# Kernel optimization log

Hardware: AMD Instinct MI355X
Metric: run time of the kernel (lower is better)

The kernel has to match this reference:

```python
import jax, jax.numpy as jnp
import numpy as np
from jax import lax

C = 41  # class_size
B = 1024
T = 1024

def setup_inputs() -> dict:
    key = jax.random.key(0)
    k1, k2, k3, k4 = jax.random.split(key, 4)
    x = jax.random.normal(k1, (B, T, C), dtype=jnp.float32)
    # torchcrf initializes transitions uniform in [-0.1, 0.1]
    start_transitions = jax.random.uniform(k2, (C,), minval=-0.1, maxval=0.1, dtype=jnp.float32)
    end_transitions = jax.random.uniform(k3, (C,), minval=-0.1, maxval=0.1, dtype=jnp.float32)
    transitions = jax.random.uniform(k4, (C, C), minval=-0.1, maxval=0.1, dtype=jnp.float32)
    return {"x": x, "start_transitions": start_transitions,
            "end_transitions": end_transitions, "transitions": transitions}

def reference(x, start_transitions, end_transitions, transitions):
    # Viterbi decode (torchcrf CRF.decode, batch_first, no mask).
    # x: [B, T, C] emissions. Returns best tag sequence [B, T] int32.
    emis_t = jnp.swapaxes(x, 0, 1)  # [T, B, C]
    score0 = start_transitions[None, :] + emis_t[0]  # [B, C]

    def fwd_step(score, emit):
        # score [B, C] (prev tag), emit [B, C] (next tag)
        # next_score[b, i, j] = score[b, i] + trans[i, j] + emit[b, j]
        ns = score[:, :, None] + transitions[None, :, :] + emit[:, None, :]
        best_prev = jnp.argmax(ns, axis=1).astype(jnp.int32)  # [B, C]
        return jnp.max(ns, axis=1), best_prev

    final_score, history = lax.scan(fwd_step, score0, emis_t[1:])  # history [T-1, B, C]
    final_score = final_score + end_transitions[None, :]
    last_tag = jnp.argmax(final_score, axis=1).astype(jnp.int32)  # [B]

    def back_step(tag, idx_t):
        # idx_t [B, C]: best previous tag given current tag
        prev = jnp.take_along_axis(idx_t, tag[:, None], axis=1)[:, 0]
        return prev, prev

    _, tags_prefix = lax.scan(back_step, last_tag, history, reverse=True)  # [T-1, B]
    tags = jnp.concatenate([tags_prefix, last_tag[None, :]], axis=0)  # [T, B]
    return jnp.swapaxes(tags, 0, 1)  # [B, T]
```

## Files before the change

### kernel.cpp

```cpp
#include <hip/hip_runtime.h>
#include <stdint.h>

#define NCLASS 41
#define TLEN   1024
#define NBATCH 1024
#define BP_STRIDE 41944
#define NTRANS (NCLASS * NCLASS)
#define NEGINF (-3.0e38f)
#define MASK41 ((1ull << NCLASS) - 1)

__device__ __forceinline__ float wave_max_bcast(float x) {
    int xi = __float_as_int(x);
    int t;
    t = __builtin_amdgcn_update_dpp(xi, xi, 0x111, 0xf, 0xf, false);
    x = fmaxf(x, __int_as_float(t)); xi = __float_as_int(x);
    t = __builtin_amdgcn_update_dpp(xi, xi, 0x112, 0xf, 0xf, false);
    x = fmaxf(x, __int_as_float(t)); xi = __float_as_int(x);
    t = __builtin_amdgcn_update_dpp(xi, xi, 0x114, 0xf, 0xf, false);
    x = fmaxf(x, __int_as_float(t)); xi = __float_as_int(x);
    t = __builtin_amdgcn_update_dpp(xi, xi, 0x118, 0xf, 0xf, false);
    x = fmaxf(x, __int_as_float(t)); xi = __float_as_int(x);
    t = __builtin_amdgcn_update_dpp(xi, xi, 0x142, 0xf, 0xf, false);
    x = fmaxf(x, __int_as_float(t)); xi = __float_as_int(x);
    t = __builtin_amdgcn_update_dpp(xi, xi, 0x143, 0xf, 0xf, false);
    x = fmaxf(x, __int_as_float(t));
    return __int_as_float(__builtin_amdgcn_readlane(__float_as_int(x), 63));
}

#define RDLANE(v, l) __int_as_float(__builtin_amdgcn_readlane(__float_as_int(v), (l)))

__global__ __launch_bounds__(64, 1) void crf_forward(
    const float* __restrict__ x,
    const float* __restrict__ start_t,
    const float* __restrict__ end_t,
    const float* __restrict__ trans,
    uint8_t* __restrict__ bp,
    int* __restrict__ out)
{
    __shared__ float tl[NTRANS + 32];

    const int b = blockIdx.x;
    const int j = threadIdx.x;
    const int jc = (j < NCLASS) ? j : (NCLASS - 1);

    float mx = NEGINF, mn = 3.0e38f;
    for (int k = j; k < NTRANS; k += 64) {
        float v = trans[k];
        tl[k] = v;
        mx = fmaxf(mx, v);
        mn = fminf(mn, v);
    }
    __syncthreads();
    const float Dmax = wave_max_bcast(mx);
    const float Dmin = -wave_max_bcast(-mn);
    const float D = Dmax - Dmin;

    const float* xb = x + (size_t)b * TLEN * NCLASS;
    uint8_t* bpb = bp + (size_t)b * BP_STRIDE;

    float score = start_t[jc] + xb[jc];
    float thr = wave_max_bcast(score) - D;

    auto step = [&](float e, int boff) {
        unsigned long long me =
            __ballot(score >= thr) & MASK41;
        int cnt = __popcll(me);
        int i1 = __ffsll(me) - 1;
        int i2 = 63 - __clzll(me);
        float s1 = RDLANE(score, i1);
        float s2 = RDLANE(score, i2);
        float t1 = tl[i1 * NCLASS + jc];
        float t2 = tl[i2 * NCLASS + jc];
        float v1 = s1 + t1;
        float v2 = s2 + t2;
        bool c = v2 > v1;
        float best = c ? v2 : v1;
        int bidx = c ? i2 : i1;
        if (__builtin_expect(cnt >= 3, 0)) {
            unsigned long long mr =
                me & ~((1ull << i1) | (1ull << i2));
            if (__builtin_expect(cnt <= 4, 1)) {
                int i3 = __ffsll(mr) - 1;
                int i4 = 63 - __clzll(mr);
                float s3 = RDLANE(score, i3);
                float s4 = RDLANE(score, i4);
                float v3 = s3 + tl[i3 * NCLASS + jc];
                float v4 = s4 + tl[i4 * NCLASS + jc];
                best = v1; bidx = i1;
                if (v3 > best) { best = v3; bidx = i3; }
                if (v4 > best) { best = v4; bidx = i4; }
                if (v2 > best) { best = v2; bidx = i2; }
            } else {
                best = NEGINF; bidx = 0;
                unsigned long long mm = me;
                while (mm) {
                    int ic = __ffsll(mm) - 1; mm &= mm - 1;
                    float sc = RDLANE(score, ic);
                    float vc = sc + tl[ic * NCLASS + jc];
                    if (vc > best) { best = vc; bidx = ic; }
                }
            }
        }
        bpb[boff] = (uint8_t)bidx;
        score = best + e;
        thr = wave_max_bcast(score) - D;
    };

    int eoff = 1 * NCLASS + jc;
    float e0 = xb[eoff];
    float e1 = xb[eoff + NCLASS];
    float e2 = xb[eoff + 2 * NCLASS];
    float e3 = xb[eoff + 3 * NCLASS];
    eoff += 4 * NCLASS;
    int boff = jc;

    int t0 = 1;
    for (; t0 + 7 <= TLEN - 4; t0 += 4) {
        step(e0, boff);              e0 = xb[eoff];
        step(e1, boff + NCLASS);     e1 = xb[eoff + NCLASS];
        step(e2, boff + 2 * NCLASS); e2 = xb[eoff + 2 * NCLASS];
        step(e3, boff + 3 * NCLASS); e3 = xb[eoff + 3 * NCLASS];
        eoff += 4 * NCLASS;
        boff += 4 * NCLASS;
    }
    step(e0, boff);              e0 = xb[eoff];
    step(e1, boff + NCLASS);     e1 = xb[eoff + NCLASS];
    step(e2, boff + 2 * NCLASS); e2 = xb[eoff + 2 * NCLASS];
    step(e3, boff + 3 * NCLASS);
    boff += 4 * NCLASS;
    step(e0, boff);
    step(e1, boff + NCLASS);
    step(e2, boff + 2 * NCLASS);

    float fs = score + end_t[jc];
    int idx = j;
#pragma unroll
    for (int off = 32; off >= 1; off >>= 1) {
        float ov = __shfl_xor(fs, off);
        int oi = __shfl_xor(idx, off);
        if (ov > fs || (ov == fs && oi < idx)) { fs = ov; idx = oi; }
    }
    if (j == 0) out[(size_t)b * TLEN + (TLEN - 1)] = idx;
}

__global__ __launch_bounds__(1024) void crf_backtrack(
    const uint8_t* __restrict__ bp,
    int* __restrict__ out)
{
    __shared__ uint8_t bpl[BP_STRIDE];
    __shared__ int maps[16][NCLASS];
    __shared__ int entry[16];

    const int b = blockIdx.x;
    const int tid = threadIdx.x;
    const int w = tid >> 6;
    const int lane = tid & 63;

    {
        const uint32_t* src = (const uint32_t*)(bp + (size_t)b * BP_STRIDE);
        uint32_t* dst = (uint32_t*)bpl;
        for (int i = tid; i < BP_STRIDE / 4; i += 1024) dst[i] = src[i];
    }
    __syncthreads();

    const int cs = w * 64;
    const int ce = min(cs + 64, TLEN - 1);
    const int L = ce - cs;

    {
        int xx = (lane < NCLASS) ? lane : 0;
        for (int t = ce; t > cs; --t)
            xx = bpl[(t - 1) * NCLASS + xx];
        if (lane < NCLASS) maps[w][lane] = xx;
    }
    __syncthreads();

    if (tid == 0) {
        int cur = out[(size_t)b * TLEN + (TLEN - 1)];
        for (int ww = 15; ww >= 0; --ww) {
            entry[ww] = cur;
            cur = maps[ww][cur];
        }
    }
    __syncthreads();

    {
        int xx = entry[w];
        int cap = 0;
        for (int k = 0; k < L; ++k) {
            xx = bpl[(ce - 1 - k) * NCLASS + xx];
            if (k == lane) cap = xx;
        }
        if (lane < L) out[(size_t)b * TLEN + (ce - 1 - lane)] = cap;
    }
}

extern "C" void kernel_launch(void* const* d_in, const int* in_sizes, int n_in,
                              void* d_out, int out_size, void* d_ws, size_t ws_size,
                              hipStream_t stream) {
    const float* x       = (const float*)d_in[0];
    const float* start_t = (const float*)d_in[1];
    const float* end_t   = (const float*)d_in[2];
    const float* trans   = (const float*)d_in[3];
    int* out = (int*)d_out;
    uint8_t* bp = (uint8_t*)d_ws;

    crf_forward<<<NBATCH, 64, 0, stream>>>(x, start_t, end_t, trans, bp, out);
    crf_backtrack<<<NBATCH, 1024, 0, stream>>>(bp, out);
}
```

Measured before the change: 261.0 us.

## Derive next-step pruning threshold from current max and emission max off critical path

The pruning threshold for the next step is now computed from the current score's wave max plus the precomputed wave max of the upcoming emissions and a constant, so the max reduction no longer waits on the newly computed score. The emission maxima are reduced ahead of time after each prefetch. The threshold is looser, which may admit more candidates, and an epsilon is added for rounding. The candidate branching is also simplified to test the remaining mask directly instead of a popcount.

```diff
diff --git a/kernel.cpp b/kernel.cpp
--- a/kernel.cpp
+++ b/kernel.cpp
@@ -7,7 +7,10 @@
 #define BP_STRIDE 41944
 #define NTRANS (NCLASS * NCLASS)
 #define NEGINF (-3.0e38f)
+#define EPS    2.0e-3f
 #define MASK41 ((1ull << NCLASS) - 1)
+
+#define RDLANE(v, l) __int_as_float(__builtin_amdgcn_readlane(__float_as_int(v), (l)))
 
 __device__ __forceinline__ float wave_max_bcast(float x) {
     int xi = __float_as_int(x);
@@ -26,8 +29,6 @@
     x = fmaxf(x, __int_as_float(t));
     return __int_as_float(__builtin_amdgcn_readlane(__float_as_int(x), 63));
 }
-
-#define RDLANE(v, l) __int_as_float(__builtin_amdgcn_readlane(__float_as_int(v), (l)))
 
 __global__ __launch_bounds__(64, 1) void crf_forward(
     const float* __restrict__ x,
@@ -53,44 +54,44 @@
     __syncthreads();
     const float Dmax = wave_max_bcast(mx);
     const float Dmin = -wave_max_bcast(-mn);
-    const float D = Dmax - Dmin;
+    const float D  = Dmax - Dmin;
+    const float Cc = Dmin - D - EPS;
 
     const float* xb = x + (size_t)b * TLEN * NCLASS;
     uint8_t* bpb = bp + (size_t)b * BP_STRIDE;
 
     float score = start_t[jc] + xb[jc];
-    float thr = wave_max_bcast(score) - D;
-
-    auto step = [&](float e, int boff) {
-        unsigned long long me =
-            __ballot(score >= thr) & MASK41;
-        int cnt = __popcll(me);
+
+    float thr = wave_max_bcast(score) - D - EPS;
+
+    auto step = [&](float e, float E, int boff) {
+        unsigned long long me = __ballot(score >= thr) & MASK41;
         int i1 = __ffsll(me) - 1;
         int i2 = 63 - __clzll(me);
+        unsigned long long mr = me & ~((1ull << i1) | (1ull << i2));
         float s1 = RDLANE(score, i1);
         float s2 = RDLANE(score, i2);
         float t1 = tl[i1 * NCLASS + jc];
         float t2 = tl[i2 * NCLASS + jc];
-        float v1 = s1 + t1;
-        float v2 = s2 + t2;
-        bool c = v2 > v1;
-        float best = c ? v2 : v1;
+        float thrN = wave_max_bcast(score) + E + Cc;
+        float u1 = s1 + t1;
+        float u2 = s2 + t2;
+        bool c = u2 > u1;
+        float best = c ? u2 : u1;
         int bidx = c ? i2 : i1;
-        if (__builtin_expect(cnt >= 3, 0)) {
-            unsigned long long mr =
-                me & ~((1ull << i1) | (1ull << i2));
-            if (__builtin_expect(cnt <= 4, 1)) {
-                int i3 = __ffsll(mr) - 1;
-                int i4 = 63 - __clzll(mr);
-                float s3 = RDLANE(score, i3);
-                float s4 = RDLANE(score, i4);
-                float v3 = s3 + tl[i3 * NCLASS + jc];
-                float v4 = s4 + tl[i4 * NCLASS + jc];
-                best = v1; bidx = i1;
-                if (v3 > best) { best = v3; bidx = i3; }
-                if (v4 > best) { best = v4; bidx = i4; }
-                if (v2 > best) { best = v2; bidx = i2; }
-            } else {
+        if (__builtin_expect(mr != 0, 0)) {
+            int i3 = __ffsll(mr) - 1;
+            int i4 = 63 - __clzll(mr);
+            unsigned long long mr2 = mr & ~((1ull << i3) | (1ull << i4));
+            float s3 = RDLANE(score, i3);
+            float s4 = RDLANE(score, i4);
+            float u3 = s3 + tl[i3 * NCLASS + jc];
+            float u4 = s4 + tl[i4 * NCLASS + jc];
+            best = u1; bidx = i1;
+            if (u3 > best) { best = u3; bidx = i3; }
+            if (u4 > best) { best = u4; bidx = i4; }
+            if (u2 > best) { best = u2; bidx = i2; }
+            if (__builtin_expect(mr2 != 0, 0)) {
                 best = NEGINF; bidx = 0;
                 unsigned long long mm = me;
                 while (mm) {
@@ -103,7 +104,7 @@
         }
         bpb[boff] = (uint8_t)bidx;
         score = best + e;
-        thr = wave_max_bcast(score) - D;
+        thr = thrN;
     };
 
     int eoff = 1 * NCLASS + jc;
@@ -111,26 +112,30 @@
     float e1 = xb[eoff + NCLASS];
     float e2 = xb[eoff + 2 * NCLASS];
     float e3 = xb[eoff + 3 * NCLASS];
+    float E0 = wave_max_bcast(e0);
+    float E1 = wave_max_bcast(e1);
+    float E2 = wave_max_bcast(e2);
+    float E3 = wave_max_bcast(e3);
     eoff += 4 * NCLASS;
     int boff = jc;
 
     int t0 = 1;
     for (; t0 + 7 <= TLEN - 4; t0 += 4) {
-        step(e0, boff);              e0 = xb[eoff];
-        step(e1, boff + NCLASS);     e1 = xb[eoff + NCLASS];
-        step(e2, boff + 2 * NCLASS); e2 = xb[eoff + 2 * NCLASS];
-        step(e3, boff + 3 * NCLASS); e3 = xb[eoff + 3 * NCLASS];
+        step(e0, E0, boff);              e0 = xb[eoff];              E0 = wave_max_bcast(e0);
+        step(e1, E1, boff + NCLASS);     e1 = xb[eoff + NCLASS];     E1 = wave_max_bcast(e1);
+        step(e2, E2, boff + 2 * NCLASS); e2 = xb[eoff + 2 * NCLASS]; E2 = wave_max_bcast(e2);
+        step(e3, E3, boff + 3 * NCLASS); e3 = xb[eoff + 3 * NCLASS]; E3 = wave_max_bcast(e3);
         eoff += 4 * NCLASS;
         boff += 4 * NCLASS;
     }
-    step(e0, boff);              e0 = xb[eoff];
-    step(e1, boff + NCLASS);     e1 = xb[eoff + NCLASS];
-    step(e2, boff + 2 * NCLASS); e2 = xb[eoff + 2 * NCLASS];
-    step(e3, boff + 3 * NCLASS);
+    step(e0, E0, boff);              e0 = xb[eoff];              E0 = wave_max_bcast(e0);
+    step(e1, E1, boff + NCLASS);     e1 = xb[eoff + NCLASS];     E1 = wave_max_bcast(e1);
+    step(e2, E2, boff + 2 * NCLASS); e2 = xb[eoff + 2 * NCLASS]; E2 = wave_max_bcast(e2);
+    step(e3, E3, boff + 3 * NCLASS);
     boff += 4 * NCLASS;
-    step(e0, boff);
-    step(e1, boff + NCLASS);
-    step(e2, boff + 2 * NCLASS);
+    step(e0, E0, boff);
+    step(e1, E1, boff + NCLASS);
+    step(e2, E2, boff + 2 * NCLASS);
 
     float fs = score + end_t[jc];
     int idx = j;
```

After: 464.6 us. 78.0% more time.
